# Optimization experiments

Hardware: AMD Instinct MI355X
Metric: run time of the kernel (lower is better)

## Reference

```python
import jax, jax.numpy as jnp
import numpy as np

CUTOFF = 5.0
N_RBF = 20

A = 50000
F = 128
E = 500000


def setup_inputs() -> dict:
    key = jax.random.key(0)
    ks = jax.random.split(key, 10)
    return {
        "vectors": jax.random.normal(ks[0], (A, 3, F), dtype=jnp.float32),
        "scalars": jax.random.normal(ks[1], (A, 1, F), dtype=jnp.float32),
        "directions": jax.random.normal(ks[2], (E, 3), dtype=jnp.float32),
        "idx_i": jax.random.randint(ks[3], (E,), 0, A),
        "idx_j": jax.random.randint(ks[4], (E,), 0, A),
        "W1": jax.random.normal(ks[5], (F, F), dtype=jnp.float32) / np.sqrt(F),
        "b1": jnp.zeros((F,), dtype=jnp.float32),
        "W2": jax.random.normal(ks[6], (F, 3 * F), dtype=jnp.float32) / np.sqrt(F),
        "b2": jnp.zeros((3 * F,), dtype=jnp.float32),
        "Wr": jax.random.normal(ks[7], (N_RBF, 3 * F), dtype=jnp.float32) / np.sqrt(N_RBF),
        "br": jnp.zeros((3 * F,), dtype=jnp.float32),
    }


def reference(vectors, scalars, directions, idx_i, idx_j, W1, b1, W2, b2, Wr, br):
    feat = scalars.shape[-1]
    n_nodes = vectors.shape[0]
    n_rbf = Wr.shape[0]

    s = jax.nn.silu(scalars @ W1 + b1) @ W2 + b2

    # edge norms: E x 1
    norm_r = jnp.sqrt(jnp.sum(directions * directions, axis=-1, keepdims=True))

    # radial basis: sin(k*pi/rc * |r|)/|r|  -> E x n
    rr = jnp.arange(1, n_rbf + 1, dtype=directions.dtype)
    rbf = jnp.sin(rr * (jnp.pi / CUTOFF) * norm_r) / norm_r
    r = rbf @ Wr + br  # E x 3F

    # cosine cutoff with hard mask (min(delta,0)/delta == 1 inside cutoff, 0 outside)
    delta = norm_r - CUTOFF
    mask = jnp.minimum(delta, 0.0) / delta
    fc = 0.5 * (jnp.cos(jnp.pi * norm_r / CUTOFF) + 1.0) * mask
    r = fc * r  # E x 3F

    combined = s[idx_i] * r[:, None, :]
    delta_s, delta_v1, delta_v2 = jnp.split(combined, 3, axis=-1)

    delta_v = vectors[idx_i] * delta_v1 + delta_v2 * (directions / norm_r)[:, :, None]

    # scatter-add back to nodes
    delta_s = jax.ops.segment_sum(delta_s, idx_j, num_segments=n_nodes)
    delta_v = jax.ops.segment_sum(delta_v, idx_j, num_segments=n_nodes)
    return delta_v, delta_s
```

## Files before the change

### kernel.cpp

```cpp
#include <hip/hip_runtime.h>
#include <math.h>

#define A_NODES 50000
#define FEAT 128
#define EDGES 500000
#define NRBF 20
#define CUTOFF_F 5.0f
#define PI_OVER_CUTOFF 0.6283185307179586f

typedef unsigned int uint32;
typedef unsigned short ushort16;
typedef short bf16x8 __attribute__((ext_vector_type(8)));
typedef float f32x4 __attribute__((ext_vector_type(4)));
typedef float f32x2 __attribute__((ext_vector_type(2)));

__device__ __forceinline__ ushort16 f2bf(float f) {
    union { float f; uint32 u; } v; v.f = f;
    uint32 r = (v.u + 0x7fffu + ((v.u >> 16) & 1u)) >> 16;
    return (ushort16)r;
}
__device__ __forceinline__ uint32 packbf(float a, float b) {
    return (uint32)f2bf(a) | ((uint32)f2bf(b) << 16);
}
__device__ __forceinline__ float bf_lo(uint32 u) { return __uint_as_float(u << 16); }
__device__ __forceinline__ float bf_hi(uint32 u) { return __uint_as_float(u & 0xffff0000u); }

#if __has_builtin(__builtin_amdgcn_fdot2_f32_bf16)
typedef __bf16 bf16x2 __attribute__((ext_vector_type(2)));
__device__ __forceinline__ float dot2(uint32 a, uint32 b, float c) {
    return __builtin_amdgcn_fdot2_f32_bf16(
        __builtin_bit_cast(bf16x2, a), __builtin_bit_cast(bf16x2, b), c, false);
}
#else
__device__ __forceinline__ float dot2(uint32 a, uint32 b, float c) {
    return fmaf(bf_hi(a), bf_hi(b), fmaf(bf_lo(a), bf_lo(b), c));
}
#endif

__global__ __launch_bounds__(256) void pack_kernel(
    const float* __restrict__ W1, const float* __restrict__ W2,
    const float* __restrict__ Wr,
    ushort16* __restrict__ w1pk, ushort16* __restrict__ w2pk,
    uint32* __restrict__ wrpk)
{
    const int t = blockIdx.x * 256 + threadIdx.x;
    if (t < 16384) {
        const int jj = t & 7, l = (t >> 3) & 63, kk = (t >> 9) & 3, nt = t >> 11;
        const int col = (l & 15) + 16 * nt;
        const int k   = kk * 32 + (l >> 4) * 8 + jj;
        w1pk[t] = f2bf(W1[k * 128 + col]);
    } else if (t < 16384 + 49152) {
        const int u = t - 16384;
        const int jj = u & 7, l = (u >> 3) & 63, kk = (u >> 9) & 3, nt = u >> 11;
        const int col = (l & 15) + 16 * nt;
        const int k   = kk * 32 + (l >> 4) * 8 + jj;
        w2pk[u] = f2bf(W2[k * 384 + col]);
    } else if (t < 16384 + 49152 + 3840) {
        const int u = t - 16384 - 49152;
        const int m = u / 384, col = u % 384;
        wrpk[u] = packbf(Wr[(2 * m) * 384 + col], Wr[(2 * m + 1) * 384 + col]);
    }
}

__global__ __launch_bounds__(256) void node_mlp_kernel(
    const float* __restrict__ scalars,
    const ushort16* __restrict__ w1pk, const float* __restrict__ bias1,
    const ushort16* __restrict__ w2pk, const float* __restrict__ bias2,
    ushort16* __restrict__ s_bf)
{
    __shared__ ushort16 sc[16][136];
    __shared__ ushort16 hd[16][136];
    const int tx   = threadIdx.x;
    const int lane = tx & 63;
    const int wv   = tx >> 6;
    const int base = blockIdx.x * 16;

    {
        const int row = tx >> 4;
        const int cs  = (tx & 15) * 8;
        const float* src = scalars + (size_t)(base + row) * FEAT + cs;
        const float4 f0 = *(const float4*)src;
        const float4 f1 = *(const float4*)(src + 4);
        bf16x8 tmp;
        tmp[0] = (short)f2bf(f0.x); tmp[1] = (short)f2bf(f0.y);
        tmp[2] = (short)f2bf(f0.z); tmp[3] = (short)f2bf(f0.w);
        tmp[4] = (short)f2bf(f1.x); tmp[5] = (short)f2bf(f1.y);
        tmp[6] = (short)f2bf(f1.z); tmp[7] = (short)f2bf(f1.w);
        *(bf16x8*)&sc[row][cs] = tmp;
    }
    __syncthreads();

    const int arow = lane & 15;
    const int kgrp = lane >> 4;

    f32x4 acc0 = {0.f, 0.f, 0.f, 0.f};
    f32x4 acc1 = {0.f, 0.f, 0.f, 0.f};
    #pragma unroll
    for (int kk = 0; kk < 4; ++kk) {
        const bf16x8 a  = *(const bf16x8*)&sc[arow][kk * 32 + kgrp * 8];
        const bf16x8 b0 = *(const bf16x8*)(w1pk + (((size_t)(wv * 2 + 0) * 4 + kk) * 64 + lane) * 8);
        const bf16x8 b1 = *(const bf16x8*)(w1pk + (((size_t)(wv * 2 + 1) * 4 + kk) * 64 + lane) * 8);
        acc0 = __builtin_amdgcn_mfma_f32_16x16x32_bf16(a, b0, acc0, 0, 0, 0);
        acc1 = __builtin_amdgcn_mfma_f32_16x16x32_bf16(a, b1, acc1, 0, 0, 0);
    }
    {
        const int c0 = wv * 32 + (lane & 15);
        const int c1 = c0 + 16;
        const float bb0 = bias1[c0], bb1 = bias1[c1];
        #pragma unroll
        for (int r = 0; r < 4; ++r) {
            const int row = kgrp * 4 + r;
            float x0 = acc0[r] + bb0;
            float x1 = acc1[r] + bb1;
            x0 = x0 / (1.0f + __expf(-x0));
            x1 = x1 / (1.0f + __expf(-x1));
            hd[row][c0] = f2bf(x0);
            hd[row][c1] = f2bf(x1);
        }
    }
    __syncthreads();

    f32x4 acc[6];
    #pragma unroll
    for (int n = 0; n < 6; ++n) acc[n] = (f32x4){0.f, 0.f, 0.f, 0.f};
    #pragma unroll
    for (int kk = 0; kk < 4; ++kk) {
        const bf16x8 a = *(const bf16x8*)&hd[arow][kk * 32 + kgrp * 8];
        #pragma unroll
        for (int n = 0; n < 6; ++n) {
            const bf16x8 b = *(const bf16x8*)(w2pk + (((size_t)(wv * 6 + n) * 4 + kk) * 64 + lane) * 8);
            acc[n] = __builtin_amdgcn_mfma_f32_16x16x32_bf16(a, b, acc[n], 0, 0, 0);
        }
    }
    #pragma unroll
    for (int n = 0; n < 6; ++n) {
        const int col = (wv * 6 + n) * 16 + (lane & 15);
        const float bb = bias2[col];
        #pragma unroll
        for (int r = 0; r < 4; ++r) {
            const int row = kgrp * 4 + r;
            s_bf[(size_t)(base + row) * 384 + col] = f2bf(acc[n][r] + bb);
        }
    }
}

__global__ __launch_bounds__(256) void vec_cvt_kernel(
    const float* __restrict__ vin, uint4* __restrict__ vbf)
{
    const size_t t = (size_t)blockIdx.x * 256 + threadIdx.x;
    const size_t n8 = (size_t)A_NODES * 384 / 8;
    if (t < n8) {
        const float4 f0 = ((const float4*)vin)[2 * t];
        const float4 f1 = ((const float4*)vin)[2 * t + 1];
        uint4 o;
        o.x = packbf(f0.x, f0.y); o.y = packbf(f0.z, f0.w);
        o.z = packbf(f1.x, f1.y); o.w = packbf(f1.z, f1.w);
        vbf[t] = o;
    }
}

__global__ __launch_bounds__(256) void hist_kernel(
    const int* __restrict__ idx_j, int* __restrict__ hist)
{
    const int e = blockIdx.x * 256 + threadIdx.x;
    if (e < EDGES) atomicAdd(&hist[idx_j[e]], 1);
}

__global__ __launch_bounds__(1024) void scan_kernel(
    const int* __restrict__ hist, int* __restrict__ offsets,
    int* __restrict__ cursor)
{
    __shared__ int part[1024];
    const int t = threadIdx.x;
    const int CH = (A_NODES + 1023) / 1024;

    int sum = 0;
    for (int k = 0; k < CH; ++k) {
        const int idx = t * CH + k;
        if (idx < A_NODES) sum += hist[idx];
    }
    part[t] = sum;
    __syncthreads();
    for (int off = 1; off < 1024; off <<= 1) {
        const int v = (t >= off) ? part[t - off] : 0;
        __syncthreads();
        part[t] += v;
        __syncthreads();
    }
    int run = part[t] - sum;
    for (int k = 0; k < CH; ++k) {
        const int idx = t * CH + k;
        if (idx < A_NODES) {
            offsets[idx] = run;
            cursor[idx]  = run;
            run += hist[idx];
        }
    }
    if (t == 0) offsets[A_NODES] = EDGES;
}

__global__ __launch_bounds__(256) void edge_prep_kernel(
    const float* __restrict__ directions,
    const int* __restrict__ idx_i, const int* __restrict__ idx_j,
    int* __restrict__ cursor,
    float* __restrict__ edata)
{
    const int e = blockIdx.x * 256 + threadIdx.x;
    if (e >= EDGES) return;
    const int j   = idx_j[e];
    const int pos = atomicAdd(&cursor[j], 1);
    const int i   = idx_i[e];
    const float d0 = directions[(size_t)e * 3 + 0];
    const float d1 = directions[(size_t)e * 3 + 1];
    const float d2 = directions[(size_t)e * 3 + 2];
    const float nr   = sqrtf(d0 * d0 + d1 * d1 + d2 * d2);
    const float invn = 1.0f / nr;
    const float x = PI_OVER_CUTOFF * nr;
    float sx, cx;
    sincosf(x, &sx, &cx);
    const float fc = (nr < CUTOFF_F) ? 0.5f * (cx + 1.0f) : 0.0f;
    const float scale = invn * fc;
    const float twoc = 2.0f * cx;

    float out16[16];
    float s_odd = sx;
    float s_prev = 0.0f;
    #pragma unroll
    for (int m = 0; m < 10; ++m) {
        const float s_even = twoc * s_odd - s_prev;
        out16[m] = __uint_as_float(packbf(s_odd * scale, s_even * scale));
        const float s_next = twoc * s_even - s_odd;
        s_prev = s_even;
        s_odd  = s_next;
    }
    out16[10] = d0 * invn;
    out16[11] = d1 * invn;
    out16[12] = d2 * invn;
    out16[13] = fc;
    out16[14] = __int_as_float(i);
    out16[15] = 0.0f;

    float4* dst = (float4*)(edata + (size_t)pos * 16);
    dst[0] = make_float4(out16[0],  out16[1],  out16[2],  out16[3]);
    dst[1] = make_float4(out16[4],  out16[5],  out16[6],  out16[7]);
    dst[2] = make_float4(out16[8],  out16[9],  out16[10], out16[11]);
    dst[3] = make_float4(out16[12], out16[13], out16[14], out16[15]);
}

template <int VBF>
__global__ __launch_bounds__(256, 4) void gather_kernel(
    const ushort16* __restrict__ s_bf,
    const ushort16* __restrict__ v_bf,
    const float* __restrict__ vectors_f32,
    const uint32* __restrict__ wrpk, const float* __restrict__ br,
    const float* __restrict__ edata,
    const int* __restrict__ offsets,
    float* __restrict__ out_v, float* __restrict__ out_s)
{
    const int lane = threadIdx.x & 63;
    const int wv   = threadIdx.x >> 6;
    const int j    = blockIdx.x * 4 + wv;
    const int c0   = lane * 2;

#define LDW(s, m) (*(const uint2*)(wrpk + (m) * 384 + (s) * 128 + c0))
    const uint2 w00 = LDW(0,0), w01 = LDW(0,1), w02 = LDW(0,2), w03 = LDW(0,3), w04 = LDW(0,4);
    const uint2 w05 = LDW(0,5), w06 = LDW(0,6), w07 = LDW(0,7), w08 = LDW(0,8), w09 = LDW(0,9);
    const uint2 w10 = LDW(1,0), w11 = LDW(1,1), w12 = LDW(1,2), w13 = LDW(1,3), w14 = LDW(1,4);
    const uint2 w15 = LDW(1,5), w16 = LDW(1,6), w17 = LDW(1,7), w18 = LDW(1,8), w19 = LDW(1,9);
    const uint2 w20 = LDW(2,0), w21 = LDW(2,1), w22 = LDW(2,2), w23 = LDW(2,3), w24 = LDW(2,4);
    const uint2 w25 = LDW(2,5), w26 = LDW(2,6), w27 = LDW(2,7), w28 = LDW(2,8), w29 = LDW(2,9);
#undef LDW
    const float2 brv0 = *(const float2*)(br + c0);
    const float2 brv1 = *(const float2*)(br + 128 + c0);
    const float2 brv2 = *(const float2*)(br + 256 + c0);

    const int beg = offsets[j];
    const int end = offsets[j + 1];

    float accsA = 0.f, accsB = 0.f;
    float avA0 = 0.f, avA1 = 0.f, avA2 = 0.f;
    float avB0 = 0.f, avB1 = 0.f, avB2 = 0.f;

    int p = beg;
    float4 cA, cB, cC, cD;
    if (p < end) {
        const float4* s0p = (const float4*)(edata + (size_t)p * 16);
        cA = s0p[0]; cB = s0p[1]; cC = s0p[2]; cD = s0p[3];
    }

    while (p < end) {
        const int pn = p + 1;
        const int i  = __float_as_int(cD.z);

        const ushort16* srow = s_bf + (size_t)i * 384;
        const uint32 s0 = *(const uint32*)(srow + c0);
        const uint32 s1 = *(const uint32*)(srow + 128 + c0);
        const uint32 s2 = *(const uint32*)(srow + 256 + c0);

        float vA0, vB0, vA1, vB1, vA2, vB2;
        if (VBF) {
            const ushort16* vrow = v_bf + (size_t)i * 384;
            const uint32 v0 = *(const uint32*)(vrow + c0);
            const uint32 v1 = *(const uint32*)(vrow + 128 + c0);
            const uint32 v2 = *(const uint32*)(vrow + 256 + c0);
            vA0 = bf_lo(v0); vB0 = bf_hi(v0);
            vA1 = bf_lo(v1); vB1 = bf_hi(v1);
            vA2 = bf_lo(v2); vB2 = bf_hi(v2);
        } else {
            const float* vrow = vectors_f32 + (size_t)i * 384;
            vA0 = vrow[c0];       vB0 = vrow[c0 + 1];
            vA1 = vrow[128 + c0]; vB1 = vrow[129 + c0];
            vA2 = vrow[256 + c0]; vB2 = vrow[257 + c0];
        }

        const size_t pf = (size_t)(pn < end ? pn : p) * 16;
        const float4* sn = (const float4*)(edata + pf);
        const float4 nA = sn[0], nB = sn[1], nC = sn[2], nD = sn[3];

        const uint32 b0 = __float_as_uint(cA.x), b1 = __float_as_uint(cA.y);
        const uint32 b2 = __float_as_uint(cA.z), b3 = __float_as_uint(cA.w);
        const uint32 b4 = __float_as_uint(cB.x), b5 = __float_as_uint(cB.y);
        const uint32 b6 = __float_as_uint(cB.z), b7 = __float_as_uint(cB.w);
        const uint32 b8 = __float_as_uint(cC.x), b9 = __float_as_uint(cC.y);
        const float u0 = cC.z, u1 = cC.w, u2 = cD.x, fcv = cD.y;

        float rA0 = fcv * brv0.x, rB0 = fcv * brv0.y;
        float rA1 = fcv * brv1.x, rB1 = fcv * brv1.y;
        float rA2 = fcv * brv2.x, rB2 = fcv * brv2.y;

#define DOTS(bb, wa, wb, wc) \
        rA0 = dot2(bb, wa.x, rA0); rB0 = dot2(bb, wa.y, rB0); \
        rA1 = dot2(bb, wb.x, rA1); rB1 = dot2(bb, wb.y, rB1); \
        rA2 = dot2(bb, wc.x, rA2); rB2 = dot2(bb, wc.y, rB2);
        DOTS(b0, w00, w10, w20)
        DOTS(b1, w01, w11, w21)
        DOTS(b2, w02, w12, w22)
        DOTS(b3, w03, w13, w23)
        DOTS(b4, w04, w14, w24)
        DOTS(b5, w05, w15, w25)
        DOTS(b6, w06, w16, w26)
        DOTS(b7, w07, w17, w27)
        DOTS(b8, w08, w18, w28)
        DOTS(b9, w09, w19, w29)
#undef DOTS

        const float sA0 = bf_lo(s0), sB0 = bf_hi(s0);
        const float sA1 = bf_lo(s1), sB1 = bf_hi(s1);
        const float sA2 = bf_lo(s2), sB2 = bf_hi(s2);

        accsA = fmaf(sA0, rA0, accsA);
        accsB = fmaf(sB0, rB0, accsB);
        const float gA1 = sA1 * rA1, gA2 = sA2 * rA2;
        const float gB1 = sB1 * rB1, gB2 = sB2 * rB2;

        avA0 = fmaf(vA0, gA1, fmaf(gA2, u0, avA0));
        avB0 = fmaf(vB0, gB1, fmaf(gB2, u0, avB0));
        avA1 = fmaf(vA1, gA1, fmaf(gA2, u1, avA1));
        avB1 = fmaf(vB1, gB1, fmaf(gB2, u1, avB1));
        avA2 = fmaf(vA2, gA1, fmaf(gA2, u2, avA2));
        avB2 = fmaf(vB2, gB1, fmaf(gB2, u2, avB2));

        cA = nA; cB = nB; cC = nC; cD = nD;
        p = pn;
    }

    f32x2 t;
    t.x = accsA; t.y = accsB;
    __builtin_nontemporal_store(t, (f32x2*)(out_s + (size_t)j * 128 + c0));
    float* ov = out_v + (size_t)j * 384;
    t.x = avA0; t.y = avB0;
    __builtin_nontemporal_store(t, (f32x2*)(ov + c0));
    t.x = avA1; t.y = avB1;
    __builtin_nontemporal_store(t, (f32x2*)(ov + 128 + c0));
    t.x = avA2; t.y = avB2;
    __builtin_nontemporal_store(t, (f32x2*)(ov + 256 + c0));
}

extern "C" void kernel_launch(void* const* d_in, const int* in_sizes, int n_in,
                              void* d_out, int out_size, void* d_ws, size_t ws_size,
                              hipStream_t stream) {
    const float* vectors    = (const float*)d_in[0];
    const float* scalars    = (const float*)d_in[1];
    const float* directions = (const float*)d_in[2];
    const int*   idx_i      = (const int*)d_in[3];
    const int*   idx_j      = (const int*)d_in[4];
    const float* W1         = (const float*)d_in[5];
    const float* b1         = (const float*)d_in[6];
    const float* W2         = (const float*)d_in[7];
    const float* b2         = (const float*)d_in[8];
    const float* Wr         = (const float*)d_in[9];
    const float* br         = (const float*)d_in[10];

    float* out_v = (float*)d_out;
    float* out_s = out_v + (size_t)A_NODES * 3 * FEAT;

    char* ws = (char*)d_ws;
    ushort16* s_bf = (ushort16*)ws;  ws += (size_t)A_NODES * 384 * 2;
    float* edata   = (float*)ws;     ws += (size_t)EDGES * 16 * 4;
    uint32* wrpk   = (uint32*)ws;    ws += (size_t)10 * 384 * 4;
    ushort16* w1pk = (ushort16*)ws;  ws += (size_t)16384 * 2;
    ushort16* w2pk = (ushort16*)ws;  ws += (size_t)49152 * 2;
    int* hist      = (int*)ws;       ws += (size_t)A_NODES * 4;
    int* offsets   = (int*)ws;       ws += (((size_t)(A_NODES + 1) * 4 + 15) & ~(size_t)15);
    int* cursor    = (int*)ws;       ws += (size_t)A_NODES * 4;
    ushort16* v_bf = (ushort16*)ws;  ws += (size_t)A_NODES * 384 * 2;

    const int use_vbf = ((size_t)(ws - (char*)d_ws) <= ws_size) ? 1 : 0;

    hipMemsetAsync(hist, 0, (size_t)A_NODES * 4, stream);

    pack_kernel<<<271, 256, 0, stream>>>(W1, W2, Wr, w1pk, w2pk, wrpk);
    node_mlp_kernel<<<A_NODES / 16, 256, 0, stream>>>(scalars, w1pk, b1, w2pk, b2, s_bf);
    if (use_vbf)
        vec_cvt_kernel<<<(int)(((size_t)A_NODES * 384 / 8 + 255) / 256), 256, 0, stream>>>(
            vectors, (uint4*)v_bf);

    hist_kernel<<<(EDGES + 255) / 256, 256, 0, stream>>>(idx_j, hist);
    scan_kernel<<<1, 1024, 0, stream>>>(hist, offsets, cursor);
    edge_prep_kernel<<<(EDGES + 255) / 256, 256, 0, stream>>>(
        directions, idx_i, idx_j, cursor, edata);

    if (use_vbf)
        gather_kernel<1><<<A_NODES / 4, 256, 0, stream>>>(
            s_bf, v_bf, vectors, wrpk, br, edata, offsets, out_v, out_s);
    else
        gather_kernel<0><<<A_NODES / 4, 256, 0, stream>>>(
            s_bf, v_bf, vectors, wrpk, br, edata, offsets, out_v, out_s);
}
```

Measured before the change: 571.6 us.

## Software-pipeline gather loop with two-deep edge prefetch and early row gathers

```diff
diff --git a/kernel.cpp b/kernel.cpp
--- a/kernel.cpp
+++ b/kernel.cpp
@@ -240,11 +240,15 @@
     out16[14] = __int_as_float(i);
     out16[15] = 0.0f;
 
-    float4* dst = (float4*)(edata + (size_t)pos * 16);
-    dst[0] = make_float4(out16[0],  out16[1],  out16[2],  out16[3]);
-    dst[1] = make_float4(out16[4],  out16[5],  out16[6],  out16[7]);
-    dst[2] = make_float4(out16[8],  out16[9],  out16[10], out16[11]);
-    dst[3] = make_float4(out16[12], out16[13], out16[14], out16[15]);
+    f32x4* dst = (f32x4*)(edata + (size_t)pos * 16);
+    f32x4 q0 = {out16[0],  out16[1],  out16[2],  out16[3]};
+    f32x4 q1 = {out16[4],  out16[5],  out16[6],  out16[7]};
+    f32x4 q2 = {out16[8],  out16[9],  out16[10], out16[11]};
+    f32x4 q3 = {out16[12], out16[13], out16[14], out16[15]};
+    __builtin_nontemporal_store(q0, dst + 0);
+    __builtin_nontemporal_store(q1, dst + 1);
+    __builtin_nontemporal_store(q2, dst + 2);
+    __builtin_nontemporal_store(q3, dst + 3);
 }
 
 template <int VBF>
@@ -258,21 +262,9 @@
     float* __restrict__ out_v, float* __restrict__ out_s)
 {
     const int lane = threadIdx.x & 63;
-    const int wv   = threadIdx.x >> 6;
+    const int wv   = __builtin_amdgcn_readfirstlane(threadIdx.x >> 6);
     const int j    = blockIdx.x * 4 + wv;
     const int c0   = lane * 2;
-
-#define LDW(s, m) (*(const uint2*)(wrpk + (m) * 384 + (s) * 128 + c0))
-    const uint2 w00 = LDW(0,0), w01 = LDW(0,1), w02 = LDW(0,2), w03 = LDW(0,3), w04 = LDW(0,4);
-    const uint2 w05 = LDW(0,5), w06 = LDW(0,6), w07 = LDW(0,7), w08 = LDW(0,8), w09 = LDW(0,9);
-    const uint2 w10 = LDW(1,0), w11 = LDW(1,1), w12 = LDW(1,2), w13 = LDW(1,3), w14 = LDW(1,4);
-    const uint2 w15 = LDW(1,5), w16 = LDW(1,6), w17 = LDW(1,7), w18 = LDW(1,8), w19 = LDW(1,9);
-    const uint2 w20 = LDW(2,0), w21 = LDW(2,1), w22 = LDW(2,2), w23 = LDW(2,3), w24 = LDW(2,4);
-    const uint2 w25 = LDW(2,5), w26 = LDW(2,6), w27 = LDW(2,7), w28 = LDW(2,8), w29 = LDW(2,9);
-#undef LDW
-    const float2 brv0 = *(const float2*)(br + c0);
-    const float2 brv1 = *(const float2*)(br + 128 + c0);
-    const float2 brv2 = *(const float2*)(br + 256 + c0);
 
     const int beg = offsets[j];
     const int end = offsets[j + 1];
@@ -281,87 +273,155 @@
     float avA0 = 0.f, avA1 = 0.f, avA2 = 0.f;
     float avB0 = 0.f, avB1 = 0.f, avB2 = 0.f;
 
-    int p = beg;
-    float4 cA, cB, cC, cD;
-    if (p < end) {
-        const float4* s0p = (const float4*)(edata + (size_t)p * 16);
-        cA = s0p[0]; cB = s0p[1]; cC = s0p[2]; cD = s0p[3];
-    }
-
-    while (p < end) {
-        const int pn = p + 1;
-        const int i  = __float_as_int(cD.z);
-
-        const ushort16* srow = s_bf + (size_t)i * 384;
-        const uint32 s0 = *(const uint32*)(srow + c0);
-        const uint32 s1 = *(const uint32*)(srow + 128 + c0);
-        const uint32 s2 = *(const uint32*)(srow + 256 + c0);
-
-        float vA0, vB0, vA1, vB1, vA2, vB2;
+    if (beg < end) {
+#define LDW(s, m) (*(const uint2*)(wrpk + (m) * 384 + (s) * 128 + c0))
+        uint2 w00 = LDW(0,0), w01 = LDW(0,1), w02 = LDW(0,2), w03 = LDW(0,3), w04 = LDW(0,4);
+        uint2 w05 = LDW(0,5), w06 = LDW(0,6), w07 = LDW(0,7), w08 = LDW(0,8), w09 = LDW(0,9);
+        uint2 w10 = LDW(1,0), w11 = LDW(1,1), w12 = LDW(1,2), w13 = LDW(1,3), w14 = LDW(1,4);
+        uint2 w15 = LDW(1,5), w16 = LDW(1,6), w17 = LDW(1,7), w18 = LDW(1,8), w19 = LDW(1,9);
+        uint2 w20 = LDW(2,0), w21 = LDW(2,1), w22 = LDW(2,2), w23 = LDW(2,3), w24 = LDW(2,4);
+        uint2 w25 = LDW(2,5), w26 = LDW(2,6), w27 = LDW(2,7), w28 = LDW(2,8), w29 = LDW(2,9);
+#undef LDW
+        asm volatile("" : "+v"(w00.x),"+v"(w00.y),"+v"(w01.x),"+v"(w01.y),
+                          "+v"(w02.x),"+v"(w02.y),"+v"(w03.x),"+v"(w03.y),
+                          "+v"(w04.x),"+v"(w04.y),"+v"(w05.x),"+v"(w05.y),
+                          "+v"(w06.x),"+v"(w06.y),"+v"(w07.x),"+v"(w07.y),
+                          "+v"(w08.x),"+v"(w08.y),"+v"(w09.x),"+v"(w09.y));
+        asm volatile("" : "+v"(w10.x),"+v"(w10.y),"+v"(w11.x),"+v"(w11.y),
+                          "+v"(w12.x),"+v"(w12.y),"+v"(w13.x),"+v"(w13.y),
+                          "+v"(w14.x),"+v"(w14.y),"+v"(w15.x),"+v"(w15.y),
+                          "+v"(w16.x),"+v"(w16.y),"+v"(w17.x),"+v"(w17.y),
+                          "+v"(w18.x),"+v"(w18.y),"+v"(w19.x),"+v"(w19.y));
+        asm volatile("" : "+v"(w20.x),"+v"(w20.y),"+v"(w21.x),"+v"(w21.y),
+                          "+v"(w22.x),"+v"(w22.y),"+v"(w23.x),"+v"(w23.y),
+                          "+v"(w24.x),"+v"(w24.y),"+v"(w25.x),"+v"(w25.y),
+                          "+v"(w26.x),"+v"(w26.y),"+v"(w27.x),"+v"(w27.y),
+                          "+v"(w28.x),"+v"(w28.y),"+v"(w29.x),"+v"(w29.y));
+
+        const float2 brv0 = *(const float2*)(br + c0);
+        const float2 brv1 = *(const float2*)(br + 128 + c0);
+        const float2 brv2 = *(const float2*)(br + 256 + c0);
+
+        const int n = end - beg;
+
+#define ED_LOAD(A_, B_, C_, D_, IDX) { \
+        const f32x4* q_ = (const f32x4*)(edata + (size_t)(IDX) * 16); \
+        A_ = q_[0]; B_ = q_[1]; C_ = q_[2]; D_ = q_[3]; }
+
+        f32x4 cA, cB, cC, cD;
+        ED_LOAD(cA, cB, cC, cD, beg)
+        f32x4 nA, nB, nC, nD;
+        ED_LOAD(nA, nB, nC, nD, (1 < n) ? beg + 1 : beg)
+
+        int i_cur = __float_as_int(cD.z);
+        const ushort16* srow = s_bf + (size_t)i_cur * 384;
+        uint32 gs0 = *(const uint32*)(srow + c0);
+        uint32 gs1 = *(const uint32*)(srow + 128 + c0);
+        uint32 gs2 = *(const uint32*)(srow + 256 + c0);
+        uint32 gv0, gv1, gv2;
+        float  gfA0, gfB0, gfA1, gfB1, gfA2, gfB2;
         if (VBF) {
-            const ushort16* vrow = v_bf + (size_t)i * 384;
-            const uint32 v0 = *(const uint32*)(vrow + c0);
-            const uint32 v1 = *(const uint32*)(vrow + 128 + c0);
-            const uint32 v2 = *(const uint32*)(vrow + 256 + c0);
-            vA0 = bf_lo(v0); vB0 = bf_hi(v0);
-            vA1 = bf_lo(v1); vB1 = bf_hi(v1);
-            vA2 = bf_lo(v2); vB2 = bf_hi(v2);
+            const ushort16* vrow = v_bf + (size_t)i_cur * 384;
+            gv0 = *(const uint32*)(vrow + c0);
+            gv1 = *(const uint32*)(vrow + 128 + c0);
+            gv2 = *(const uint32*)(vrow + 256 + c0);
         } else {
-            const float* vrow = vectors_f32 + (size_t)i * 384;
-            vA0 = vrow[c0];       vB0 = vrow[c0 + 1];
-            vA1 = vrow[128 + c0]; vB1 = vrow[129 + c0];
-            vA2 = vrow[256 + c0]; vB2 = vrow[257 + c0];
-        }
-
-        const size_t pf = (size_t)(pn < end ? pn : p) * 16;
-        const float4* sn = (const float4*)(edata + pf);
-        const float4 nA = sn[0], nB = sn[1], nC = sn[2], nD = sn[3];
-
-        const uint32 b0 = __float_as_uint(cA.x), b1 = __float_as_uint(cA.y);
-        const uint32 b2 = __float_as_uint(cA.z), b3 = __float_as_uint(cA.w);
-        const uint32 b4 = __float_as_uint(cB.x), b5 = __float_as_uint(cB.y);
-        const uint32 b6 = __float_as_uint(cB.z), b7 = __float_as_uint(cB.w);
-        const uint32 b8 = __float_as_uint(cC.x), b9 = __float_as_uint(cC.y);
-        const float u0 = cC.z, u1 = cC.w, u2 = cD.x, fcv = cD.y;
-
-        float rA0 = fcv * brv0.x, rB0 = fcv * brv0.y;
-        float rA1 = fcv * brv1.x, rB1 = fcv * brv1.y;
-        float rA2 = fcv * brv2.x, rB2 = fcv * brv2.y;
+            const float* vrow = vectors_f32 + (size_t)i_cur * 384;
+            gfA0 = vrow[c0];       gfB0 = vrow[c0 + 1];
+            gfA1 = vrow[128 + c0]; gfB1 = vrow[129 + c0];
+            gfA2 = vrow[256 + c0]; gfB2 = vrow[257 + c0];
+        }
+
+        for (int k = 0; k < n; ++k) {
+            int idx2 = beg + k + 2;
+            if (idx2 > end - 1) idx2 = end - 1;
+            f32x4 fA, fB, fC, fD;
+            ED_LOAD(fA, fB, fC, fD, idx2)
+
+            const int i_nxt = __float_as_int(nD.z);
+            const ushort16* srow2 = s_bf + (size_t)i_nxt * 384;
+            const uint32 hs0 = *(const uint32*)(srow2 + c0);
+            const uint32 hs1 = *(const uint32*)(srow2 + 128 + c0);
+            const uint32 hs2 = *(const uint32*)(srow2 + 256 + c0);
+            uint32 hv0, hv1, hv2;
+            float  hfA0, hfB0, hfA1, hfB1, hfA2, hfB2;
+            if (VBF) {
+                const ushort16* vrow2 = v_bf + (size_t)i_nxt * 384;
+                hv0 = *(const uint32*)(vrow2 + c0);
+                hv1 = *(const uint32*)(vrow2 + 128 + c0);
+                hv2 = *(const uint32*)(vrow2 + 256 + c0);
+            } else {
+                const float* vrow2 = vectors_f32 + (size_t)i_nxt * 384;
+                hfA0 = vrow2[c0];       hfB0 = vrow2[c0 + 1];
+                hfA1 = vrow2[128 + c0]; hfB1 = vrow2[129 + c0];
+                hfA2 = vrow2[256 + c0]; hfB2 = vrow2[257 + c0];
+            }
+
+            const uint32 b0 = __float_as_uint(cA.x), b1 = __float_as_uint(cA.y);
+            const uint32 b2 = __float_as_uint(cA.z), b3 = __float_as_uint(cA.w);
+            const uint32 b4 = __float_as_uint(cB.x), b5 = __float_as_uint(cB.y);
+            const uint32 b6 = __float_as_uint(cB.z), b7 = __float_as_uint(cB.w);
+            const uint32 b8 = __float_as_uint(cC.x), b9 = __float_as_uint(cC.y);
+            const float u0 = cC.z, u1 = cC.w, u2 = cD.x, fcv = cD.y;
+
+            float rA0 = fcv * brv0.x, rB0 = fcv * brv0.y;
+            float rA1 = fcv * brv1.x, rB1 = fcv * brv1.y;
+            float rA2 = fcv * brv2.x, rB2 = fcv * brv2.y;
 
 #define DOTS(bb, wa, wb, wc) \
-        rA0 = dot2(bb, wa.x, rA0); rB0 = dot2(bb, wa.y, rB0); \
-        rA1 = dot2(bb, wb.x, rA1); rB1 = dot2(bb, wb.y, rB1); \
-        rA2 = dot2(bb, wc.x, rA2); rB2 = dot2(bb, wc.y, rB2);
-        DOTS(b0, w00, w10, w20)
-        DOTS(b1, w01, w11, w21)
-        DOTS(b2, w02, w12, w22)
-        DOTS(b3, w03, w13, w23)
-        DOTS(b4, w04, w14, w24)
-        DOTS(b5, w05, w15, w25)
-        DOTS(b6, w06, w16, w26)
-        DOTS(b7, w07, w17, w27)
-        DOTS(b8, w08, w18, w28)
-        DOTS(b9, w09, w19, w29)
+            rA0 = dot2(bb, wa.x, rA0); rB0 = dot2(bb, wa.y, rB0); \
+            rA1 = dot2(bb, wb.x, rA1); rB1 = dot2(bb, wb.y, rB1); \
+            rA2 = dot2(bb, wc.x, rA2); rB2 = dot2(bb, wc.y, rB2);
+            DOTS(b0, w00, w10, w20)
+            DOTS(b1, w01, w11, w21)
+            DOTS(b2, w02, w12, w22)
+            DOTS(b3, w03, w13, w23)
+            DOTS(b4, w04, w14, w24)
+            DOTS(b5, w05, w15, w25)
+            DOTS(b6, w06, w16, w26)
+            DOTS(b7, w07, w17, w27)
+            DOTS(b8, w08, w18, w28)
+            DOTS(b9, w09, w19, w29)
 #undef DOTS
 
-        const float sA0 = bf_lo(s0), sB0 = bf_hi(s0);
-        const float sA1 = bf_lo(s1), sB1 = bf_hi(s1);
-        const float sA2 = bf_lo(s2), sB2 = bf_hi(s2);
-
-        accsA = fmaf(sA0, rA0, accsA);
-        accsB = fmaf(sB0, rB0, accsB);
-        const float gA1 = sA1 * rA1, gA2 = sA2 * rA2;
-        const float gB1 = sB1 * rB1, gB2 = sB2 * rB2;
-
-        avA0 = fmaf(vA0, gA1, fmaf(gA2, u0, avA0));
-        avB0 = fmaf(vB0, gB1, fmaf(gB2, u0, avB0));
-        avA1 = fmaf(vA1, gA1, fmaf(gA2, u1, avA1));
-        avB1 = fmaf(vB1, gB1, fmaf(gB2, u1, avB1));
-        avA2 = fmaf(vA2, gA1, fmaf(gA2, u2, avA2));
-        avB2 = fmaf(vB2, gB1, fmaf(gB2, u2, avB2));
-
-        cA = nA; cB = nB; cC = nC; cD = nD;
-        p = pn;
+            const float sA0 = bf_lo(gs0), sB0 = bf_hi(gs0);
+            const float sA1 = bf_lo(gs1), sB1 = bf_hi(gs1);
+            const float sA2 = bf_lo(gs2), sB2 = bf_hi(gs2);
+
+            accsA = fmaf(sA0, rA0, accsA);
+            accsB = fmaf(sB0, rB0, accsB);
+            const float gA1 = sA1 * rA1, gA2 = sA2 * rA2;
+            const float gB1 = sB1 * rB1, gB2 = sB2 * rB2;
+
+            float vA0, vB0, vA1, vB1, vA2, vB2;
+            if (VBF) {
+                vA0 = bf_lo(gv0); vB0 = bf_hi(gv0);
+                vA1 = bf_lo(gv1); vB1 = bf_hi(gv1);
+                vA2 = bf_lo(gv2); vB2 = bf_hi(gv2);
+            } else {
+                vA0 = gfA0; vB0 = gfB0;
+                vA1 = gfA1; vB1 = gfB1;
+                vA2 = gfA2; vB2 = gfB2;
+            }
+
+            avA0 = fmaf(vA0, gA1, fmaf(gA2, u0, avA0));
+            avB0 = fmaf(vB0, gB1, fmaf(gB2, u0, avB0));
+            avA1 = fmaf(vA1, gA1, fmaf(gA2, u1, avA1));
+            avB1 = fmaf(vB1, gB1, fmaf(gB2, u1, avB1));
+            avA2 = fmaf(vA2, gA1, fmaf(gA2, u2, avA2));
+            avB2 = fmaf(vB2, gB1, fmaf(gB2, u2, avB2));
+
+            cA = nA; cB = nB; cC = nC; cD = nD;
+            nA = fA; nB = fB; nC = fC; nD = fD;
+            gs0 = hs0; gs1 = hs1; gs2 = hs2;
+            if (VBF) { gv0 = hv0; gv1 = hv1; gv2 = hv2; }
+            else {
+                gfA0 = hfA0; gfB0 = hfB0;
+                gfA1 = hfA1; gfB1 = hfB1;
+                gfA2 = hfA2; gfB2 = hfB2;
+            }
+        }
+#undef ED_LOAD
     }
 
     f32x2 t;
```

Result: slower. 593.1 us (+3.8%).

## Split gather work across three waves per node and merge prep kernels

Applied to the files above, without the earlier changes.

```diff
diff --git a/kernel.cpp b/kernel.cpp
--- a/kernel.cpp
+++ b/kernel.cpp
@@ -37,28 +37,52 @@
 }
 #endif
 
-__global__ __launch_bounds__(256) void pack_kernel(
+#define NB_CVT 9375
+#define NB_HIST 1954
+#define NB_PACK 271
+
+__global__ __launch_bounds__(256) void prep_kernel(
+    const float* __restrict__ vin, uint4* __restrict__ vbf, int use_vbf,
+    const int* __restrict__ idx_j, int* __restrict__ hist,
     const float* __restrict__ W1, const float* __restrict__ W2,
     const float* __restrict__ Wr,
     ushort16* __restrict__ w1pk, ushort16* __restrict__ w2pk,
     uint32* __restrict__ wrpk)
 {
-    const int t = blockIdx.x * 256 + threadIdx.x;
-    if (t < 16384) {
-        const int jj = t & 7, l = (t >> 3) & 63, kk = (t >> 9) & 3, nt = t >> 11;
-        const int col = (l & 15) + 16 * nt;
-        const int k   = kk * 32 + (l >> 4) * 8 + jj;
-        w1pk[t] = f2bf(W1[k * 128 + col]);
-    } else if (t < 16384 + 49152) {
-        const int u = t - 16384;
-        const int jj = u & 7, l = (u >> 3) & 63, kk = (u >> 9) & 3, nt = u >> 11;
-        const int col = (l & 15) + 16 * nt;
-        const int k   = kk * 32 + (l >> 4) * 8 + jj;
-        w2pk[u] = f2bf(W2[k * 384 + col]);
-    } else if (t < 16384 + 49152 + 3840) {
-        const int u = t - 16384 - 49152;
-        const int m = u / 384, col = u % 384;
-        wrpk[u] = packbf(Wr[(2 * m) * 384 + col], Wr[(2 * m + 1) * 384 + col]);
+    const int b = blockIdx.x;
+    if (b < NB_CVT) {
+        if (!use_vbf) return;
+        const size_t t = (size_t)b * 256 + threadIdx.x;
+        const size_t n8 = (size_t)A_NODES * 384 / 8;
+        if (t < n8) {
+            const float4 f0 = ((const float4*)vin)[2 * t];
+            const float4 f1 = ((const float4*)vin)[2 * t + 1];
+            uint4 o;
+            o.x = packbf(f0.x, f0.y); o.y = packbf(f0.z, f0.w);
+            o.z = packbf(f1.x, f1.y); o.w = packbf(f1.z, f1.w);
+            vbf[t] = o;
+        }
+    } else if (b < NB_CVT + NB_HIST) {
+        const int e = (b - NB_CVT) * 256 + threadIdx.x;
+        if (e < EDGES) atomicAdd(&hist[idx_j[e]], 1);
+    } else {
+        const int t = (b - NB_CVT - NB_HIST) * 256 + threadIdx.x;
+        if (t < 16384) {
+            const int jj = t & 7, l = (t >> 3) & 63, kk = (t >> 9) & 3, nt = t >> 11;
+            const int col = (l & 15) + 16 * nt;
+            const int k   = kk * 32 + (l >> 4) * 8 + jj;
+            w1pk[t] = f2bf(W1[k * 128 + col]);
+        } else if (t < 16384 + 49152) {
+            const int u = t - 16384;
+            const int jj = u & 7, l = (u >> 3) & 63, kk = (u >> 9) & 3, nt = u >> 11;
+            const int col = (l & 15) + 16 * nt;
+            const int k   = kk * 32 + (l >> 4) * 8 + jj;
+            w2pk[u] = f2bf(W2[k * 384 + col]);
+        } else if (t < 16384 + 49152 + 3840) {
+            const int u = t - 16384 - 49152;
+            const int m = u / 384, col = u % 384;
+            wrpk[u] = packbf(Wr[(2 * m) * 384 + col], Wr[(2 * m + 1) * 384 + col]);
+        }
     }
 }
 
@@ -142,28 +166,6 @@
             s_bf[(size_t)(base + row) * 384 + col] = f2bf(acc[n][r] + bb);
         }
     }
-}
-
-__global__ __launch_bounds__(256) void vec_cvt_kernel(
-    const float* __restrict__ vin, uint4* __restrict__ vbf)
-{
-    const size_t t = (size_t)blockIdx.x * 256 + threadIdx.x;
-    const size_t n8 = (size_t)A_NODES * 384 / 8;
-    if (t < n8) {
-        const float4 f0 = ((const float4*)vin)[2 * t];
-        const float4 f1 = ((const float4*)vin)[2 * t + 1];
-        uint4 o;
-        o.x = packbf(f0.x, f0.y); o.y = packbf(f0.z, f0.w);
-        o.z = packbf(f1.x, f1.y); o.w = packbf(f1.z, f1.w);
-        vbf[t] = o;
-    }
-}
-
-__global__ __launch_bounds__(256) void hist_kernel(
-    const int* __restrict__ idx_j, int* __restrict__ hist)
-{
-    const int e = blockIdx.x * 256 + threadIdx.x;
-    if (e < EDGES) atomicAdd(&hist[idx_j[e]], 1);
 }
 
 __global__ __launch_bounds__(1024) void scan_kernel(
@@ -240,15 +242,19 @@
     out16[14] = __int_as_float(i);
     out16[15] = 0.0f;
 
-    float4* dst = (float4*)(edata + (size_t)pos * 16);
-    dst[0] = make_float4(out16[0],  out16[1],  out16[2],  out16[3]);
-    dst[1] = make_float4(out16[4],  out16[5],  out16[6],  out16[7]);
-    dst[2] = make_float4(out16[8],  out16[9],  out16[10], out16[11]);
-    dst[3] = make_float4(out16[12], out16[13], out16[14], out16[15]);
+    f32x4* dst = (f32x4*)(edata + (size_t)pos * 16);
+    f32x4 q0 = {out16[0],  out16[1],  out16[2],  out16[3]};
+    f32x4 q1 = {out16[4],  out16[5],  out16[6],  out16[7]};
+    f32x4 q2 = {out16[8],  out16[9],  out16[10], out16[11]};
+    f32x4 q3 = {out16[12], out16[13], out16[14], out16[15]};
+    __builtin_nontemporal_store(q0, dst + 0);
+    __builtin_nontemporal_store(q1, dst + 1);
+    __builtin_nontemporal_store(q2, dst + 2);
+    __builtin_nontemporal_store(q3, dst + 3);
 }
 
 template <int VBF>
-__global__ __launch_bounds__(256, 4) void gather_kernel(
+__global__ __launch_bounds__(384, 6) void gather_kernel(
     const ushort16* __restrict__ s_bf,
     const ushort16* __restrict__ v_bf,
     const float* __restrict__ vectors_f32,
@@ -258,122 +264,144 @@
     float* __restrict__ out_v, float* __restrict__ out_s)
 {
     const int lane = threadIdx.x & 63;
-    const int wv   = threadIdx.x >> 6;
-    const int j    = blockIdx.x * 4 + wv;
+    const int wv   = __builtin_amdgcn_readfirstlane(threadIdx.x >> 6);
+    const int nsub = wv / 3;
+    const int seg  = wv % 3;
+    const int j    = blockIdx.x * 2 + nsub;
     const int c0   = lane * 2;
-
-#define LDW(s, m) (*(const uint2*)(wrpk + (m) * 384 + (s) * 128 + c0))
-    const uint2 w00 = LDW(0,0), w01 = LDW(0,1), w02 = LDW(0,2), w03 = LDW(0,3), w04 = LDW(0,4);
-    const uint2 w05 = LDW(0,5), w06 = LDW(0,6), w07 = LDW(0,7), w08 = LDW(0,8), w09 = LDW(0,9);
-    const uint2 w10 = LDW(1,0), w11 = LDW(1,1), w12 = LDW(1,2), w13 = LDW(1,3), w14 = LDW(1,4);
-    const uint2 w15 = LDW(1,5), w16 = LDW(1,6), w17 = LDW(1,7), w18 = LDW(1,8), w19 = LDW(1,9);
-    const uint2 w20 = LDW(2,0), w21 = LDW(2,1), w22 = LDW(2,2), w23 = LDW(2,3), w24 = LDW(2,4);
-    const uint2 w25 = LDW(2,5), w26 = LDW(2,6), w27 = LDW(2,7), w28 = LDW(2,8), w29 = LDW(2,9);
+    const int soff = seg * 128 + c0;
+
+#define LDW(m) (*(const uint2*)(wrpk + (m) * 384 + soff))
+    uint2 w0 = LDW(0), w1 = LDW(1), w2 = LDW(2), w3 = LDW(3), w4 = LDW(4);
+    uint2 w5 = LDW(5), w6 = LDW(6), w7 = LDW(7), w8 = LDW(8), w9 = LDW(9);
 #undef LDW
-    const float2 brv0 = *(const float2*)(br + c0);
-    const float2 brv1 = *(const float2*)(br + 128 + c0);
-    const float2 brv2 = *(const float2*)(br + 256 + c0);
+    asm volatile("" : "+v"(w0.x),"+v"(w0.y),"+v"(w1.x),"+v"(w1.y),
+                      "+v"(w2.x),"+v"(w2.y),"+v"(w3.x),"+v"(w3.y),
+                      "+v"(w4.x),"+v"(w4.y),"+v"(w5.x),"+v"(w5.y),
+                      "+v"(w6.x),"+v"(w6.y),"+v"(w7.x),"+v"(w7.y),
+                      "+v"(w8.x),"+v"(w8.y),"+v"(w9.x),"+v"(w9.y));
+    const float2 brv = *(const float2*)(br + soff);
 
     const int beg = offsets[j];
     const int end = offsets[j + 1];
 
-    float accsA = 0.f, accsB = 0.f;
-    float avA0 = 0.f, avA1 = 0.f, avA2 = 0.f;
-    float avB0 = 0.f, avB1 = 0.f, avB2 = 0.f;
-
-    int p = beg;
-    float4 cA, cB, cC, cD;
-    if (p < end) {
-        const float4* s0p = (const float4*)(edata + (size_t)p * 16);
-        cA = s0p[0]; cB = s0p[1]; cC = s0p[2]; cD = s0p[3];
-    }
-
-    while (p < end) {
-        const int pn = p + 1;
-        const int i  = __float_as_int(cD.z);
-
-        const ushort16* srow = s_bf + (size_t)i * 384;
-        const uint32 s0 = *(const uint32*)(srow + c0);
-        const uint32 s1 = *(const uint32*)(srow + 128 + c0);
-        const uint32 s2 = *(const uint32*)(srow + 256 + c0);
-
-        float vA0, vB0, vA1, vB1, vA2, vB2;
-        if (VBF) {
-            const ushort16* vrow = v_bf + (size_t)i * 384;
-            const uint32 v0 = *(const uint32*)(vrow + c0);
-            const uint32 v1 = *(const uint32*)(vrow + 128 + c0);
-            const uint32 v2 = *(const uint32*)(vrow + 256 + c0);
-            vA0 = bf_lo(v0); vB0 = bf_hi(v0);
-            vA1 = bf_lo(v1); vB1 = bf_hi(v1);
-            vA2 = bf_lo(v2); vB2 = bf_hi(v2);
-        } else {
-            const float* vrow = vectors_f32 + (size_t)i * 384;
-            vA0 = vrow[c0];       vB0 = vrow[c0 + 1];
-            vA1 = vrow[128 + c0]; vB1 = vrow[129 + c0];
-            vA2 = vrow[256 + c0]; vB2 = vrow[257 + c0];
-        }
-
-        const size_t pf = (size_t)(pn < end ? pn : p) * 16;
-        const float4* sn = (const float4*)(edata + pf);
-        const float4 nA = sn[0], nB = sn[1], nC = sn[2], nD = sn[3];
-
-        const uint32 b0 = __float_as_uint(cA.x), b1 = __float_as_uint(cA.y);
-        const uint32 b2 = __float_as_uint(cA.z), b3 = __float_as_uint(cA.w);
-        const uint32 b4 = __float_as_uint(cB.x), b5 = __float_as_uint(cB.y);
-        const uint32 b6 = __float_as_uint(cB.z), b7 = __float_as_uint(cB.w);
-        const uint32 b8 = __float_as_uint(cC.x), b9 = __float_as_uint(cC.y);
-        const float u0 = cC.z, u1 = cC.w, u2 = cD.x, fcv = cD.y;
-
-        float rA0 = fcv * brv0.x, rB0 = fcv * brv0.y;
-        float rA1 = fcv * brv1.x, rB1 = fcv * brv1.y;
-        float rA2 = fcv * brv2.x, rB2 = fcv * brv2.y;
-
-#define DOTS(bb, wa, wb, wc) \
-        rA0 = dot2(bb, wa.x, rA0); rB0 = dot2(bb, wa.y, rB0); \
-        rA1 = dot2(bb, wb.x, rA1); rB1 = dot2(bb, wb.y, rB1); \
-        rA2 = dot2(bb, wc.x, rA2); rB2 = dot2(bb, wc.y, rB2);
-        DOTS(b0, w00, w10, w20)
-        DOTS(b1, w01, w11, w21)
-        DOTS(b2, w02, w12, w22)
-        DOTS(b3, w03, w13, w23)
-        DOTS(b4, w04, w14, w24)
-        DOTS(b5, w05, w15, w25)
-        DOTS(b6, w06, w16, w26)
-        DOTS(b7, w07, w17, w27)
-        DOTS(b8, w08, w18, w28)
-        DOTS(b9, w09, w19, w29)
-#undef DOTS
-
-        const float sA0 = bf_lo(s0), sB0 = bf_hi(s0);
-        const float sA1 = bf_lo(s1), sB1 = bf_hi(s1);
-        const float sA2 = bf_lo(s2), sB2 = bf_hi(s2);
-
-        accsA = fmaf(sA0, rA0, accsA);
-        accsB = fmaf(sB0, rB0, accsB);
-        const float gA1 = sA1 * rA1, gA2 = sA2 * rA2;
-        const float gB1 = sB1 * rB1, gB2 = sB2 * rB2;
-
-        avA0 = fmaf(vA0, gA1, fmaf(gA2, u0, avA0));
-        avB0 = fmaf(vB0, gB1, fmaf(gB2, u0, avB0));
-        avA1 = fmaf(vA1, gA1, fmaf(gA2, u1, avA1));
-        avB1 = fmaf(vB1, gB1, fmaf(gB2, u1, avB1));
-        avA2 = fmaf(vA2, gA1, fmaf(gA2, u2, avA2));
-        avB2 = fmaf(vB2, gB1, fmaf(gB2, u2, avB2));
-
-        cA = nA; cB = nB; cC = nC; cD = nD;
-        p = pn;
-    }
-
-    f32x2 t;
-    t.x = accsA; t.y = accsB;
-    __builtin_nontemporal_store(t, (f32x2*)(out_s + (size_t)j * 128 + c0));
-    float* ov = out_v + (size_t)j * 384;
-    t.x = avA0; t.y = avB0;
-    __builtin_nontemporal_store(t, (f32x2*)(ov + c0));
-    t.x = avA1; t.y = avB1;
-    __builtin_nontemporal_store(t, (f32x2*)(ov + 128 + c0));
-    t.x = avA2; t.y = avB2;
-    __builtin_nontemporal_store(t, (f32x2*)(ov + 256 + c0));
+    f32x2 acc = {0.f, 0.f};
+    f32x2 av0 = {0.f, 0.f}, av1 = {0.f, 0.f}, av2 = {0.f, 0.f};
+
+    if (beg < end) {
+        int i_c = __float_as_int(edata[(size_t)beg * 16 + 14]);
+        uint32 s_c = *(const uint32*)(s_bf + (size_t)i_c * 384 + soff);
+        uint32 vb0_c = 0, vb1_c = 0, vb2_c = 0;
+        f32x2  vf0_c = {0,0}, vf1_c = {0,0}, vf2_c = {0,0};
+        if (seg == 1) {
+            if (VBF) {
+                const ushort16* vrow = v_bf + (size_t)i_c * 384;
+                vb0_c = *(const uint32*)(vrow + c0);
+                vb1_c = *(const uint32*)(vrow + 128 + c0);
+                vb2_c = *(const uint32*)(vrow + 256 + c0);
+            } else {
+                const float* vrow = vectors_f32 + (size_t)i_c * 384;
+                vf0_c = *(const f32x2*)(vrow + c0);
+                vf1_c = *(const f32x2*)(vrow + 128 + c0);
+                vf2_c = *(const f32x2*)(vrow + 256 + c0);
+            }
+        }
+
+        for (int p = beg; p < end; ++p) {
+            const int pn = (p + 1 < end) ? p + 1 : p;
+            const int i_n = __float_as_int(edata[(size_t)pn * 16 + 14]);
+            const uint32 s_n = *(const uint32*)(s_bf + (size_t)i_n * 384 + soff);
+            uint32 vb0_n = 0, vb1_n = 0, vb2_n = 0;
+            f32x2  vf0_n = {0,0}, vf1_n = {0,0}, vf2_n = {0,0};
+            if (seg == 1) {
+                if (VBF) {
+                    const ushort16* vrow = v_bf + (size_t)i_n * 384;
+                    vb0_n = *(const uint32*)(vrow + c0);
+                    vb1_n = *(const uint32*)(vrow + 128 + c0);
+                    vb2_n = *(const uint32*)(vrow + 256 + c0);
+                } else {
+                    const float* vrow = vectors_f32 + (size_t)i_n * 384;
+                    vf0_n = *(const f32x2*)(vrow + c0);
+                    vf1_n = *(const f32x2*)(vrow + 128 + c0);
+                    vf2_n = *(const f32x2*)(vrow + 256 + c0);
+                }
+            }
+
+            const float* ed = edata + (size_t)p * 16;
+            const uint32 b0 = __float_as_uint(ed[0]), b1 = __float_as_uint(ed[1]);
+            const uint32 b2 = __float_as_uint(ed[2]), b3 = __float_as_uint(ed[3]);
+            const uint32 b4 = __float_as_uint(ed[4]), b5 = __float_as_uint(ed[5]);
+            const uint32 b6 = __float_as_uint(ed[6]), b7 = __float_as_uint(ed[7]);
+            const uint32 b8 = __float_as_uint(ed[8]), b9 = __float_as_uint(ed[9]);
+            const float fcv = ed[13];
+
+            float rA = fcv * brv.x, rB = fcv * brv.y;
+            rA = dot2(b0, w0.x, rA); rB = dot2(b0, w0.y, rB);
+            rA = dot2(b1, w1.x, rA); rB = dot2(b1, w1.y, rB);
+            rA = dot2(b2, w2.x, rA); rB = dot2(b2, w2.y, rB);
+            rA = dot2(b3, w3.x, rA); rB = dot2(b3, w3.y, rB);
+            rA = dot2(b4, w4.x, rA); rB = dot2(b4, w4.y, rB);
+            rA = dot2(b5, w5.x, rA); rB = dot2(b5, w5.y, rB);
+            rA = dot2(b6, w6.x, rA); rB = dot2(b6, w6.y, rB);
+            rA = dot2(b7, w7.x, rA); rB = dot2(b7, w7.y, rB);
+            rA = dot2(b8, w8.x, rA); rB = dot2(b8, w8.y, rB);
+            rA = dot2(b9, w9.x, rA); rB = dot2(b9, w9.y, rB);
+
+            const float gA = bf_lo(s_c) * rA;
+            const float gB = bf_hi(s_c) * rB;
+
+            if (seg == 0) {
+                acc.x += gA; acc.y += gB;
+            } else if (seg == 1) {
+                float vA0, vB0, vA1, vB1, vA2, vB2;
+                if (VBF) {
+                    vA0 = bf_lo(vb0_c); vB0 = bf_hi(vb0_c);
+                    vA1 = bf_lo(vb1_c); vB1 = bf_hi(vb1_c);
+                    vA2 = bf_lo(vb2_c); vB2 = bf_hi(vb2_c);
+                } else {
+                    vA0 = vf0_c.x; vB0 = vf0_c.y;
+                    vA1 = vf1_c.x; vB1 = vf1_c.y;
+                    vA2 = vf2_c.x; vB2 = vf2_c.y;
+                }
+                av0.x = fmaf(gA, vA0, av0.x); av0.y = fmaf(gB, vB0, av0.y);
+                av1.x = fmaf(gA, vA1, av1.x); av1.y = fmaf(gB, vB1, av1.y);
+                av2.x = fmaf(gA, vA2, av2.x); av2.y = fmaf(gB, vB2, av2.y);
+            } else {
+                const float u0 = ed[10], u1 = ed[11], u2 = ed[12];
+                av0.x = fmaf(gA, u0, av0.x); av0.y = fmaf(gB, u0, av0.y);
+                av1.x = fmaf(gA, u1, av1.x); av1.y = fmaf(gB, u1, av1.y);
+                av2.x = fmaf(gA, u2, av2.x); av2.y = fmaf(gB, u2, av2.y);
+            }
+
+            s_c = s_n;
+            vb0_c = vb0_n; vb1_c = vb1_n; vb2_c = vb2_n;
+            vf0_c = vf0_n; vf1_c = vf1_n; vf2_c = vf2_n;
+        }
+    }
+
+    __shared__ f32x2 red[2][64][3];
+    if (seg == 2) {
+        red[nsub][lane][0] = av0;
+        red[nsub][lane][1] = av1;
+        red[nsub][lane][2] = av2;
+    }
+    __syncthreads();
+
+    if (seg == 0) {
+        __builtin_nontemporal_store(acc, (f32x2*)(out_s + (size_t)j * 128 + c0));
+    } else if (seg == 1) {
+        const f32x2 o0 = red[nsub][lane][0];
+        const f32x2 o1 = red[nsub][lane][1];
+        const f32x2 o2 = red[nsub][lane][2];
+        float* ov = out_v + (size_t)j * 384;
+        f32x2 t;
+        t.x = av0.x + o0.x; t.y = av0.y + o0.y;
+        __builtin_nontemporal_store(t, (f32x2*)(ov + c0));
+        t.x = av1.x + o1.x; t.y = av1.y + o1.y;
+        __builtin_nontemporal_store(t, (f32x2*)(ov + 128 + c0));
+        t.x = av2.x + o2.x; t.y = av2.y + o2.y;
+        __builtin_nontemporal_store(t, (f32x2*)(ov + 256 + c0));
+    }
 }
 
 extern "C" void kernel_launch(void* const* d_in, const int* in_sizes, int n_in,
@@ -409,21 +437,19 @@
 
     hipMemsetAsync(hist, 0, (size_t)A_NODES * 4, stream);
 
-    pack_kernel<<<271, 256, 0, stream>>>(W1, W2, Wr, w1pk, w2pk, wrpk);
+    prep_kernel<<<NB_CVT + NB_HIST + NB_PACK, 256, 0, stream>>>(
+        vectors, (uint4*)v_bf, use_vbf, idx_j, hist,
+        W1, W2, Wr, w1pk, w2pk, wrpk);
+
     node_mlp_kernel<<<A_NODES / 16, 256, 0, stream>>>(scalars, w1pk, b1, w2pk, b2, s_bf);
-    if (use_vbf)
-        vec_cvt_kernel<<<(int)(((size_t)A_NODES * 384 / 8 + 255) / 256), 256, 0, stream>>>(
-            vectors, (uint4*)v_bf);
-
-    hist_kernel<<<(EDGES + 255) / 256, 256, 0, stream>>>(idx_j, hist);
     scan_kernel<<<1, 1024, 0, stream>>>(hist, offsets, cursor);
     edge_prep_kernel<<<(EDGES + 255) / 256, 256, 0, stream>>>(
         directions, idx_i, idx_j, cursor, edata);
 
     if (use_vbf)
-        gather_kernel<1><<<A_NODES / 4, 256, 0, stream>>>(
+        gather_kernel<1><<<A_NODES / 2, 384, 0, stream>>>(
             s_bf, v_bf, vectors, wrpk, br, edata, offsets, out_v, out_s);
     else
-        gather_kernel<0><<<A_NODES / 4, 256, 0, stream>>>(
+        gather_kernel<0><<<A_NODES / 2, 384, 0, stream>>>(
             s_bf, v_bf, vectors, wrpk, br, edata, offsets, out_v, out_s);
 }
```

Result: slower. 653.2 us (+14.3%).
